# Kernel optimization log

Measured on AMD Instinct MI355X. Metric: run time of the kernel, lower is better.

## Reference

```python
import jax, jax.numpy as jnp
import numpy as np

D_MODEL = 1024
N_HEADS = 16
HEAD_DIM = D_MODEL // N_HEADS
D_LATENT = 256
LAMBDA_DECAY = 0.01
TIME_STEP = 0.01  # get_timestamps spacing; wall-clock base cancels in diffs
CLAMP = 1e4


def setup_inputs() -> dict:
    key = jax.random.key(0)
    ks = jax.random.split(key, 8)
    B, S = 2, 2048
    def w(k, i, o):
        return jax.random.normal(k, (i, o), dtype=jnp.float32) * 0.02
    return {
        "x": jax.random.normal(ks[0], (B, S, D_MODEL), dtype=jnp.float32),
        "Wq": w(ks[1], D_MODEL, D_MODEL),
        "Wk": w(ks[2], D_MODEL, D_MODEL),
        "Wv": w(ks[3], D_MODEL, D_MODEL),
        "Wo": w(ks[4], D_MODEL, D_MODEL),
        "W_down_kv": w(ks[5], D_MODEL, D_LATENT),
        "W_up_k": w(ks[6], D_LATENT, D_MODEL),
        "W_up_v": w(ks[7], D_LATENT, D_MODEL),
    }


def reference(x, Wq, Wk, Wv, Wo, W_down_kv, W_up_k, W_up_v):
    B, S, _ = x.shape
    q = x @ Wq
    k = x @ Wk
    v = x @ Wv
    latent_kv = (k + v) @ W_down_kv            # [B,S,d_latent]
    k_rec = latent_kv @ W_up_k                 # [B,S,d_model]
    v_rec = latent_kv @ W_up_v
    # split heads -> [B,H,S,hd]
    def heads(t):
        return t.reshape(B, S, N_HEADS, HEAD_DIM).transpose(0, 2, 1, 3)
    qh, kh, vh = heads(q), heads(k_rec), heads(v_rec)
    scale = 1.0 / (jnp.sqrt(jnp.float32(D_MODEL)) + 1e-8)
    scores = jnp.einsum("bhqd,bhkd->bhqk", qh, kh) * scale
    scores = jnp.clip(jnp.nan_to_num(scores, nan=-1e9), -CLAMP, CLAMP)
    # time decay: |t_i - t_j| = TIME_STEP * |i - j| (wall-clock base cancels)
    idx = jnp.arange(S, dtype=jnp.float32)
    decay = jnp.exp(-LAMBDA_DECAY * TIME_STEP * jnp.abs(idx[:, None] - idx[None, :]))
    scores = scores * decay[None, None, :, :]
    scores = jnp.clip(jnp.nan_to_num(scores, nan=-1e9), -CLAMP, CLAMP)
    attn = jax.nn.softmax(scores, axis=-1)
    out = jnp.einsum("bhqk,bhkd->bhqd", attn, vh)
    out = out.transpose(0, 2, 1, 3).reshape(B, S, D_MODEL)
    return out @ Wo, latent_kv
```

## Files before the change

### kernel.cpp

```cpp
#include <hip/hip_runtime.h>
#include <hip/hip_bf16.h>
#include <cstdint>
#include <cstddef>

typedef __bf16 bf16;
typedef __bf16 bf16x8 __attribute__((ext_vector_type(8)));
typedef float f32x4 __attribute__((ext_vector_type(4)));

#define NB 2
#define SEQ 2048
#define DM 1024
#define MTOK 4096
#define DL 256
#define NH 16
#define HD 64

#define LOG2E 1.4426950408889634f

__device__ __forceinline__ void gload16(const void* g, void* l) {
  __builtin_amdgcn_global_load_lds((const __attribute__((address_space(1))) void*)g,
                                   (__attribute__((address_space(3))) void*)l, 16, 0, 0);
}
__device__ __forceinline__ float fast_exp2(float x) {
#if __has_builtin(__builtin_amdgcn_exp2f)
  return __builtin_amdgcn_exp2f(x);
#else
  float r; asm("v_exp_f32 %0, %1" : "=v"(r) : "v"(x)); return r;
#endif
}
__device__ __forceinline__ int xcd_swz(int orig, int nwg) {
  int x = orig & 7;
  int q = nwg >> 3, r = nwg & 7;
  int base = (x < r) ? x * (q + 1) : r * (q + 1) + (x - r) * q;
  return base + (orig >> 3);
}

__device__ __forceinline__ void transpose_dev(const float* __restrict__ in0,
                                              bf16* __restrict__ out, int R, int C,
                                              int c0, int r0, int tid, float (*tile)[33]) {
  int tx = tid & 31, ty = tid >> 5;
#pragma unroll
  for (int i = 0; i < 4; ++i) {
    int r = r0 + ty + 8 * i;
    tile[ty + 8 * i][tx] = in0[(size_t)r * C + c0 + tx];
  }
  __syncthreads();
  int c = tid >> 3, s = tid & 7;
  bf16 o4[4] __attribute__((aligned(8)));
#pragma unroll
  for (int j = 0; j < 4; ++j) o4[j] = (bf16)tile[4 * s + j][c];
  *reinterpret_cast<uint2*>(out + (size_t)(c0 + c) * R + r0 + 4 * s) =
      *reinterpret_cast<const uint2*>(o4);
}

__device__ __forceinline__ void cvt8_dev(const float* __restrict__ in, bf16* __restrict__ out,
                                         int blk, int tid) {
  int i = (blk * 256 + tid) * 8;
  float4 a = *reinterpret_cast<const float4*>(in + i);
  float4 b = *reinterpret_cast<const float4*>(in + i + 4);
  bf16 o[8] __attribute__((aligned(16)));
  o[0] = (bf16)a.x; o[1] = (bf16)a.y; o[2] = (bf16)a.z; o[3] = (bf16)a.w;
  o[4] = (bf16)b.x; o[5] = (bf16)b.y; o[6] = (bf16)b.z; o[7] = (bf16)b.w;
  *reinterpret_cast<uint4*>(out + i) = *reinterpret_cast<const uint4*>(o);
}

__device__ __forceinline__ void sum8_dev(const float* __restrict__ in0, const float* __restrict__ in1,
                                         bf16* __restrict__ out, int blk, int tid) {
  int i = (blk * 256 + tid) * 8;
  float4 a0 = *reinterpret_cast<const float4*>(in0 + i);
  float4 b0 = *reinterpret_cast<const float4*>(in0 + i + 4);
  float4 a1 = *reinterpret_cast<const float4*>(in1 + i);
  float4 b1 = *reinterpret_cast<const float4*>(in1 + i + 4);
  bf16 o[8] __attribute__((aligned(16)));
  o[0] = (bf16)(a0.x + a1.x); o[1] = (bf16)(a0.y + a1.y);
  o[2] = (bf16)(a0.z + a1.z); o[3] = (bf16)(a0.w + a1.w);
  o[4] = (bf16)(b0.x + b1.x); o[5] = (bf16)(b0.y + b1.y);
  o[6] = (bf16)(b0.z + b1.z); o[7] = (bf16)(b0.w + b1.w);
  *reinterpret_cast<uint4*>(out + i) = *reinterpret_cast<const uint4*>(o);
}

__global__ __launch_bounds__(256) void prep_kernel(const float* __restrict__ x,
                                                   const float* __restrict__ Wq,
                                                   const float* __restrict__ Wk,
                                                   const float* __restrict__ Wv,
                                                   const float* __restrict__ Wo,
                                                   const float* __restrict__ Wdn,
                                                   const float* __restrict__ Wuk,
                                                   const float* __restrict__ Wuv,
                                                   bf16* xbf, bf16* WqT, bf16* WoT, bf16* WdnT,
                                                   bf16* WukT, bf16* WuvT, bf16* Wkv) {
  __shared__ float tile[32][33];
  int id = blockIdx.x, tid = threadIdx.x;
  if (id < 2048) { cvt8_dev(x, xbf, id, tid); return; }
  id -= 2048;
  if (id < 512) { sum8_dev(Wk, Wv, Wkv, id, tid); return; }
  id -= 512;
  if (id < 1024) { transpose_dev(Wq, WqT, 1024, 1024, (id & 31) * 32, (id >> 5) * 32, tid, tile); return; }
  id -= 1024;
  if (id < 1024) { transpose_dev(Wo, WoT, 1024, 1024, (id & 31) * 32, (id >> 5) * 32, tid, tile); return; }
  id -= 1024;
  if (id < 256) { transpose_dev(Wdn, WdnT, 1024, 256, (id & 7) * 32, (id >> 3) * 32, tid, tile); return; }
  id -= 256;
  if (id < 256) { transpose_dev(Wuk, WukT, 256, 1024, (id & 31) * 32, (id >> 5) * 32, tid, tile); return; }
  id -= 256;
  transpose_dev(Wuv, WuvT, 256, 1024, (id & 31) * 32, (id >> 5) * 32, tid, tile);
}

template <int EPI>
__device__ __forceinline__ void gemm_core(const bf16* __restrict__ A, const bf16* __restrict__ Bt,
                                          bf16* __restrict__ O1, float* __restrict__ Of,
                                          int K, int bx, int by, bf16* As, bf16* Bs) {
  const int tid = threadIdx.x;
  const int lane = tid & 63;
  const int wv = tid >> 6;
  const int wr = wv >> 1, wc = wv & 1;
  const int row0 = bx * 128, col0 = by * 64;
  const int l15 = lane & 15;
  const int lg = lane >> 4;

  const int r0 = tid >> 3;
  const int ccs = (tid & 7) ^ (r0 & 7);
  const bf16* aS = A + (size_t)(row0 + r0) * K + ccs * 8;
  const bf16* bS = Bt + (size_t)(col0 + r0) * K + ccs * 8;
  const int dA = tid * 8;

#pragma unroll
  for (int i = 0; i < 4; ++i) gload16(aS + (size_t)(32 * i) * K, As + dA + 2048 * i);
#pragma unroll
  for (int j = 0; j < 2; ++j) gload16(bS + (size_t)(32 * j) * K, Bs + dA + 2048 * j);
  aS += 64; bS += 64;

  int aoff[4][2], boff[2][2];
#pragma unroll
  for (int m = 0; m < 4; ++m) {
    int ra = wr * 64 + m * 16 + l15;
#pragma unroll
    for (int kk = 0; kk < 2; ++kk)
      aoff[m][kk] = ra * 64 + (((kk * 4 + lg) ^ (ra & 7)) * 8);
  }
#pragma unroll
  for (int n = 0; n < 2; ++n) {
    int rb = wc * 32 + n * 16 + l15;
#pragma unroll
    for (int kk = 0; kk < 2; ++kk)
      boff[n][kk] = rb * 64 + (((kk * 4 + lg) ^ (rb & 7)) * 8);
  }

  f32x4 acc[4][2] = {};
  int cur = 0;
  for (int k0 = 0; k0 < K; k0 += 64) {
    __syncthreads();
    if (k0 + 64 < K) {
      const int nxA = (cur ^ 1) * 8192, nxB = (cur ^ 1) * 4096;
#pragma unroll
      for (int i = 0; i < 4; ++i) gload16(aS + (size_t)(32 * i) * K, As + nxA + dA + 2048 * i);
#pragma unroll
      for (int j = 0; j < 2; ++j) gload16(bS + (size_t)(32 * j) * K, Bs + nxB + dA + 2048 * j);
      aS += 64; bS += 64;
    }
    const bf16* Ab = As + cur * 8192;
    const bf16* Bb = Bs + cur * 4096;
    bf16x8 af[4][2], bfr[2][2];
#pragma unroll
    for (int m = 0; m < 4; ++m)
#pragma unroll
      for (int kk = 0; kk < 2; ++kk)
        af[m][kk] = *reinterpret_cast<const bf16x8*>(&Ab[aoff[m][kk]]);
#pragma unroll
    for (int n = 0; n < 2; ++n)
#pragma unroll
      for (int kk = 0; kk < 2; ++kk)
        bfr[n][kk] = *reinterpret_cast<const bf16x8*>(&Bb[boff[n][kk]]);
    __builtin_amdgcn_s_setprio(1);
#pragma unroll
    for (int kk = 0; kk < 2; ++kk)
#pragma unroll
      for (int m = 0; m < 4; ++m)
#pragma unroll
        for (int n = 0; n < 2; ++n)
          acc[m][n] = __builtin_amdgcn_mfma_f32_16x16x32_bf16(af[m][kk], bfr[n][kk], acc[m][n], 0, 0, 0);
    __builtin_amdgcn_s_setprio(0);
    cur ^= 1;
  }

  const int rbase = row0 + wr * 64 + (lane >> 4) * 4;
  const int cbase = col0 + wc * 32 + l15;
#pragma unroll
  for (int m = 0; m < 4; ++m) {
#pragma unroll
    for (int n = 0; n < 2; ++n) {
      const int cc = cbase + n * 16;
      if constexpr (EPI == 0) {
#pragma unroll
        for (int r = 0; r < 4; ++r)
          O1[(size_t)(rbase + m * 16 + r) * DM + cc] = (bf16)acc[m][n][r];
      } else if constexpr (EPI == 3) {
#pragma unroll
        for (int r = 0; r < 4; ++r)
          Of[(size_t)(rbase + m * 16 + r) * DM + cc] = acc[m][n][r];
      } else {
#pragma unroll
        for (int r = 0; r < 4; ++r)
          O1[(size_t)(rbase + m * 16 + r) * MTOK + cc] = (bf16)acc[m][n][r];
      }
    }
  }
}

__device__ __forceinline__ void gemm64_lat(const bf16* __restrict__ A, const bf16* __restrict__ Bt,
                                           bf16* __restrict__ O1, float* __restrict__ Of,
                                           int K, int bx, int by, bf16* As, bf16* Bs) {
  const int tid = threadIdx.x;
  const int lane = tid & 63;
  const int wv = tid >> 6;
  const int wr = wv >> 1, wc = wv & 1;
  const int row0 = bx * 64, col0 = by * 64;
  const int l15 = lane & 15;
  const int lg = lane >> 4;

  const int r0 = tid >> 3;
  const int ccs = (tid & 7) ^ (r0 & 7);
  const bf16* aS = A + (size_t)(row0 + r0) * K + ccs * 8;
  const bf16* bS = Bt + (size_t)(col0 + r0) * K + ccs * 8;
  const int dA = tid * 8;

#pragma unroll
  for (int j = 0; j < 2; ++j) {
    gload16(aS + (size_t)(32 * j) * K, As + dA + 2048 * j);
    gload16(bS + (size_t)(32 * j) * K, Bs + dA + 2048 * j);
  }
  aS += 64; bS += 64;

  int aoff[2][2], boff[2][2];
#pragma unroll
  for (int m = 0; m < 2; ++m) {
    int ra = wr * 32 + m * 16 + l15;
    int rb = wc * 32 + m * 16 + l15;
#pragma unroll
    for (int kk = 0; kk < 2; ++kk) {
      aoff[m][kk] = ra * 64 + (((kk * 4 + lg) ^ (ra & 7)) * 8);
      boff[m][kk] = rb * 64 + (((kk * 4 + lg) ^ (rb & 7)) * 8);
    }
  }

  f32x4 acc[2][2] = {};
  int cur = 0;
  for (int k0 = 0; k0 < K; k0 += 64) {
    __syncthreads();
    if (k0 + 64 < K) {
      const int nx = (cur ^ 1) * 4096;
#pragma unroll
      for (int j = 0; j < 2; ++j) {
        gload16(aS + (size_t)(32 * j) * K, As + nx + dA + 2048 * j);
        gload16(bS + (size_t)(32 * j) * K, Bs + nx + dA + 2048 * j);
      }
      aS += 64; bS += 64;
    }
    const bf16* Ab = As + cur * 4096;
    const bf16* Bb = Bs + cur * 4096;
    bf16x8 af[2][2], bfr[2][2];
#pragma unroll
    for (int m = 0; m < 2; ++m)
#pragma unroll
      for (int kk = 0; kk < 2; ++kk) {
        af[m][kk] = *reinterpret_cast<const bf16x8*>(&Ab[aoff[m][kk]]);
        bfr[m][kk] = *reinterpret_cast<const bf16x8*>(&Bb[boff[m][kk]]);
      }
    __builtin_amdgcn_s_setprio(1);
#pragma unroll
    for (int kk = 0; kk < 2; ++kk)
#pragma unroll
      for (int m = 0; m < 2; ++m)
#pragma unroll
        for (int n = 0; n < 2; ++n)
          acc[m][n] = __builtin_amdgcn_mfma_f32_16x16x32_bf16(af[m][kk], bfr[n][kk], acc[m][n], 0, 0, 0);
    __builtin_amdgcn_s_setprio(0);
    cur ^= 1;
  }

  const int rbase = row0 + wr * 32 + (lane >> 4) * 4;
  const int cbase = col0 + wc * 32 + l15;
#pragma unroll
  for (int m = 0; m < 2; ++m)
#pragma unroll
    for (int n = 0; n < 2; ++n)
#pragma unroll
      for (int r = 0; r < 4; ++r) {
        float v = acc[m][n][r];
        O1[(size_t)(rbase + m * 16 + r) * DL + (cbase + n * 16)] = (bf16)v;
        Of[(size_t)(rbase + m * 16 + r) * DL + (cbase + n * 16)] = v;
      }
}

__global__ __launch_bounds__(256) void gemm_q_w(const bf16* __restrict__ xbf,
                                                const bf16* __restrict__ WqT, bf16* qbf,
                                                const bf16* __restrict__ WdnT,
                                                const bf16* __restrict__ Wkv, bf16* WkvdT) {
  __shared__ __align__(16) bf16 As[2 * 8192];
  __shared__ __align__(16) bf16 Bs[2 * 4096];
  int id = xcd_swz(blockIdx.x, 544);
  if (id < 32)
    gemm_core<0>(WdnT, Wkv, WkvdT, nullptr, DM, id >> 4, id & 15, As, Bs);
  else {
    int j = id - 32;
    gemm_core<0>(xbf, WqT, qbf, nullptr, DM, j >> 4, j & 15, As, Bs);
  }
}

__global__ __launch_bounds__(256) void gemm_latent(const bf16* __restrict__ xbf,
                                                   const bf16* __restrict__ WkvdT,
                                                   bf16* latbf, float* out_lat) {
  __shared__ __align__(16) bf16 As[2 * 4096];
  __shared__ __align__(16) bf16 Bs[2 * 4096];
  int id = xcd_swz(blockIdx.x, 256);
  gemm64_lat(xbf, WkvdT, latbf, out_lat, DM, id >> 2, id & 3, As, Bs);
}

__global__ __launch_bounds__(256) void gemm_up(const bf16* __restrict__ latbf,
                                               const bf16* __restrict__ WukT,
                                               const bf16* __restrict__ WuvT,
                                               bf16* kbuf, bf16* vT) {
  __shared__ __align__(16) bf16 As[2 * 8192];
  __shared__ __align__(16) bf16 Bs[2 * 4096];
  int id = xcd_swz(blockIdx.x, 1024);
  if (id < 512)
    gemm_core<0>(latbf, WukT, kbuf, nullptr, DL, id >> 4, id & 15, As, Bs);
  else {
    int j = id - 512;
    gemm_core<7>(WuvT, latbf, vT, nullptr, DL, j >> 6, j & 63, As, Bs);
  }
}

__global__ __launch_bounds__(256) void gemm_out(const bf16* __restrict__ ctx,
                                                const bf16* __restrict__ WoT, float* out0) {
  __shared__ __align__(16) bf16 As[2 * 8192];
  __shared__ __align__(16) bf16 Bs[2 * 4096];
  int id = xcd_swz(blockIdx.x, 512);
  gemm_core<3>(ctx, WoT, nullptr, out0, DM, id >> 4, id & 15, As, Bs);
}

__global__ __launch_bounds__(512) void attn_kernel(const bf16* __restrict__ Q,
                                                   const bf16* __restrict__ Kr,
                                                   const bf16* __restrict__ Vt,
                                                   bf16* __restrict__ Ctx) {
  __shared__ __align__(16) bf16 Ks[2 * 4096];
  __shared__ __align__(16) bf16 Vs[2 * 4096];
  __shared__ __align__(16) bf16 Ps[8192];
  const int work = xcd_swz(blockIdx.x, SEQ / 128 * NH * NB);
  const int qt = work & 15, h = (work >> 4) & 15, b = work >> 8;
  const int tid = threadIdx.x, lane = tid & 63, wv = tid >> 6;
  const int l15 = lane & 15, lg = lane >> 4;
  const int qbase = qt * 128 + wv * 16;
  const size_t tok0 = (size_t)b * SEQ;

  bf16x8 qf[2];
  {
    const bf16* qp = Q + (tok0 + qbase + l15) * DM + h * HD + lg * 8;
    qf[0] = *reinterpret_cast<const bf16x8*>(qp);
    qf[1] = *reinterpret_cast<const bf16x8*>(qp + 32);
  }

  const int r0s = tid >> 3;
  const int cc0 = (tid & 7) ^ (r0s & 7);
  const bf16* kS0 = Kr + (tok0 + r0s) * DM + h * HD + cc0 * 8;
  const bf16* vS0 = Vt + (size_t)(h * HD + r0s) * MTOK + tok0 + cc0 * 8;
  const int d0 = tid * 8;

  gload16(kS0, Ks + d0);
  gload16(vS0, Vs + d0);
  kS0 += 64 * DM; vS0 += 64;

  int koff[2][4], poffw[4], poffr[2];
  const int hsw = l15 & 7;
#pragma unroll
  for (int ks = 0; ks < 2; ++ks)
#pragma unroll
    for (int nf = 0; nf < 4; ++nf) {
      int row = nf * 16 + l15;
      koff[ks][nf] = row * 64 + (((ks * 4 + lg) ^ (row & 7)) * 8);
    }
  const int psBase = wv * 1024 + l15 * 64;
#pragma unroll
  for (int nf = 0; nf < 4; ++nf)
    poffw[nf] = psBase + (((nf * 2 + (lg >> 1)) ^ hsw) * 8) + (lg & 1) * 4;
#pragma unroll
  for (int ks = 0; ks < 2; ++ks)
    poffr[ks] = psBase + (((ks * 4 + lg) ^ hsw) * 8);

  bf16x8 ones;
#pragma unroll
  for (int j = 0; j < 8; ++j) ones[j] = (bf16)1.0f;

  f32x4 oacc[4] = {};
  f32x4 lacc = {};
  float dec[4][4];
  const float DEC2C = (1.0f / 32.0f) * LOG2E;
  const float NC2 = -1.0e-4f * LOG2E;
  const float E64 = 0.99362048f, IE64 = 1.00642051f;
  const int ib = -qbase - l15 + lg * 4;

  int cur = 0;
  for (int t = 0; t < SEQ / 64; ++t) {
    const int key0 = t * 64;
    __syncthreads();
    if (t + 1 < SEQ / 64) {
      const int nx = (cur ^ 1) * 4096;
      gload16(kS0, Ks + nx + d0);
      gload16(vS0, Vs + nx + d0);
      kS0 += 64 * DM; vS0 += 64;
    }
    {
      bool before = (key0 + 63 < qbase);
      bool afterp = (key0 >= qbase + 79);
      if (t == 0 || (!before && !afterp)) {
#pragma unroll
        for (int nf = 0; nf < 4; ++nf)
#pragma unroll
          for (int r = 0; r < 4; ++r) {
            float df = (float)(key0 + ib + nf * 16 + r);
            dec[nf][r] = DEC2C * fast_exp2(NC2 * fabsf(df));
          }
      } else {
        float mlt = before ? IE64 : E64;
#pragma unroll
        for (int nf = 0; nf < 4; ++nf)
#pragma unroll
          for (int r = 0; r < 4; ++r) dec[nf][r] *= mlt;
      }
    }
    const int kb = cur * 4096;

    f32x4 sc[4] = {};
    __builtin_amdgcn_s_setprio(1);
#pragma unroll
    for (int ks = 0; ks < 2; ++ks)
#pragma unroll
      for (int nf = 0; nf < 4; ++nf) {
        bf16x8 kf = *reinterpret_cast<const bf16x8*>(&Ks[kb + koff[ks][nf]]);
        sc[nf] = __builtin_amdgcn_mfma_f32_16x16x32_bf16(kf, qf[ks], sc[nf], 0, 0, 0);
      }
    __builtin_amdgcn_s_setprio(0);

#pragma unroll
    for (int nf = 0; nf < 4; ++nf) {
      bf16 t4[4] __attribute__((aligned(8)));
#pragma unroll
      for (int r = 0; r < 4; ++r) t4[r] = (bf16)fast_exp2(sc[nf][r] * dec[nf][r]);
      *reinterpret_cast<uint2*>(&Ps[poffw[nf]]) = *reinterpret_cast<const uint2*>(t4);
    }
    bf16x8 pb[2];
    pb[0] = *reinterpret_cast<const bf16x8*>(&Ps[poffr[0]]);
    pb[1] = *reinterpret_cast<const bf16x8*>(&Ps[poffr[1]]);

    __builtin_amdgcn_s_setprio(1);
#pragma unroll
    for (int ks = 0; ks < 2; ++ks) {
#pragma unroll
      for (int nf = 0; nf < 4; ++nf) {
        bf16x8 vf = *reinterpret_cast<const bf16x8*>(&Vs[kb + koff[ks][nf]]);
        oacc[nf] = __builtin_amdgcn_mfma_f32_16x16x32_bf16(vf, pb[ks], oacc[nf], 0, 0, 0);
      }
      lacc = __builtin_amdgcn_mfma_f32_16x16x32_bf16(ones, pb[ks], lacc, 0, 0, 0);
    }
    __builtin_amdgcn_s_setprio(0);
    cur ^= 1;
  }

  const float inv = 1.0f / lacc[0];
#pragma unroll
  for (int nf = 0; nf < 4; ++nf) {
    bf16 o4[4] __attribute__((aligned(8)));
#pragma unroll
    for (int r = 0; r < 4; ++r) o4[r] = (bf16)(oacc[nf][r] * inv);
    *reinterpret_cast<uint2*>(Ctx + (tok0 + qbase + l15) * DM + h * HD + nf * 16 + lg * 4) =
        *reinterpret_cast<const uint2*>(o4);
  }
}

extern "C" void kernel_launch(void* const* d_in, const int* in_sizes, int n_in,
                              void* d_out, int out_size, void* d_ws, size_t ws_size,
                              hipStream_t stream) {
  const float* x   = (const float*)d_in[0];
  const float* Wq  = (const float*)d_in[1];
  const float* Wk  = (const float*)d_in[2];
  const float* Wv  = (const float*)d_in[3];
  const float* Wo  = (const float*)d_in[4];
  const float* Wdn = (const float*)d_in[5];
  const float* Wuk = (const float*)d_in[6];
  const float* Wuv = (const float*)d_in[7];
  float* out0 = (float*)d_out;
  float* out_lat = out0 + (size_t)MTOK * DM;

  char* ws = (char*)d_ws;
  const size_t MB = 1u << 20;
  bf16* xbf   = (bf16*)(ws + 0);
  bf16* qbf   = (bf16*)(ws + 8 * MB);
  bf16* kbuf  = (bf16*)(ws + 16 * MB);
  bf16* Wkv   = kbuf;
  bf16* WkvdT = (bf16*)(ws + 18 * MB);
  bf16* vT    = (bf16*)(ws + 24 * MB);
  bf16* latbf = (bf16*)(ws + 32 * MB);
  bf16* WqT   = (bf16*)(ws + 34 * MB);
  bf16* WoT   = (bf16*)(ws + 36 * MB);
  bf16* WukT  = (bf16*)(ws + 38 * MB);
  bf16* WuvT  = (bf16*)(ws + 38 * MB + 512 * 1024);
  bf16* WdnT  = (bf16*)(ws + 39 * MB);
  bf16* ctx   = xbf;

  prep_kernel<<<5376, 256, 0, stream>>>(x, Wq, Wk, Wv, Wo, Wdn, Wuk, Wuv,
                                        xbf, WqT, WoT, WdnT, WukT, WuvT, Wkv);
  gemm_q_w<<<544, 256, 0, stream>>>(xbf, WqT, qbf, WdnT, Wkv, WkvdT);
  gemm_latent<<<256, 256, 0, stream>>>(xbf, WkvdT, latbf, out_lat);
  gemm_up<<<1024, 256, 0, stream>>>(latbf, WukT, WuvT, kbuf, vT);
  attn_kernel<<<512, 512, 0, stream>>>(qbf, kbuf, vT, ctx);
  gemm_out<<<512, 256, 0, stream>>>(ctx, WoT, out0);

  (void)in_sizes; (void)n_in; (void)out_size; (void)ws_size;
}
```

Before: 115.4 us.

## Fuse Q and latent projections into one GEMM over concatenated weights; 64x64 transposes

WkvdT is now written directly after WqT in the workspace, so a single 128x64-tile GEMM over 1280 output columns produces both Q and the latent. Its epilogue sends columns past 1024 to the bf16 latent and fp32 latent outputs. The small Wdn·Wkv product moves to its own 32-block launch ahead of it, which serializes a poorly occupied kernel that previously ran alongside the Q GEMM. The weight transposes in prep switch to 64x64 tiles with float4 loads and 16-byte stores, reducing block count and giving wider memory accesses.

```diff
diff --git a/kernel.cpp b/kernel.cpp
--- a/kernel.cpp
+++ b/kernel.cpp
@@ -35,22 +35,27 @@
   return base + (orig >> 3);
 }
 
-__device__ __forceinline__ void transpose_dev(const float* __restrict__ in0,
-                                              bf16* __restrict__ out, int R, int C,
-                                              int c0, int r0, int tid, float (*tile)[33]) {
-  int tx = tid & 31, ty = tid >> 5;
+__device__ __forceinline__ void transpose64_dev(const float* __restrict__ in0,
+                                                bf16* __restrict__ out, int R, int C,
+                                                int c0, int r0, int tid, float (*tile)[65]) {
+  int tx = tid & 15, ty = tid >> 4;
 #pragma unroll
   for (int i = 0; i < 4; ++i) {
-    int r = r0 + ty + 8 * i;
-    tile[ty + 8 * i][tx] = in0[(size_t)r * C + c0 + tx];
+    int r = r0 + ty + 16 * i;
+    float4 v = *reinterpret_cast<const float4*>(in0 + (size_t)r * C + c0 + tx * 4);
+    tile[ty + 16 * i][tx * 4 + 0] = v.x;
+    tile[ty + 16 * i][tx * 4 + 1] = v.y;
+    tile[ty + 16 * i][tx * 4 + 2] = v.z;
+    tile[ty + 16 * i][tx * 4 + 3] = v.w;
   }
   __syncthreads();
-  int c = tid >> 3, s = tid & 7;
-  bf16 o4[4] __attribute__((aligned(8)));
-#pragma unroll
-  for (int j = 0; j < 4; ++j) o4[j] = (bf16)tile[4 * s + j][c];
-  *reinterpret_cast<uint2*>(out + (size_t)(c0 + c) * R + r0 + 4 * s) =
-      *reinterpret_cast<const uint2*>(o4);
+  int c = tid >> 2, s = tid & 3;
+  bf16 o16[16] __attribute__((aligned(16)));
+#pragma unroll
+  for (int m = 0; m < 16; ++m) o16[m] = (bf16)tile[s * 16 + m][c];
+  uint4* dst = reinterpret_cast<uint4*>(out + (size_t)(c0 + c) * R + r0 + s * 16);
+  dst[0] = *reinterpret_cast<const uint4*>(o16);
+  dst[1] = *reinterpret_cast<const uint4*>(o16 + 8);
 }
 
 __device__ __forceinline__ void cvt8_dev(const float* __restrict__ in, bf16* __restrict__ out,
@@ -89,26 +94,27 @@
                                                    const float* __restrict__ Wuv,
                                                    bf16* xbf, bf16* WqT, bf16* WoT, bf16* WdnT,
                                                    bf16* WukT, bf16* WuvT, bf16* Wkv) {
-  __shared__ float tile[32][33];
+  __shared__ float tile[64][65];
   int id = blockIdx.x, tid = threadIdx.x;
   if (id < 2048) { cvt8_dev(x, xbf, id, tid); return; }
   id -= 2048;
   if (id < 512) { sum8_dev(Wk, Wv, Wkv, id, tid); return; }
   id -= 512;
-  if (id < 1024) { transpose_dev(Wq, WqT, 1024, 1024, (id & 31) * 32, (id >> 5) * 32, tid, tile); return; }
-  id -= 1024;
-  if (id < 1024) { transpose_dev(Wo, WoT, 1024, 1024, (id & 31) * 32, (id >> 5) * 32, tid, tile); return; }
-  id -= 1024;
-  if (id < 256) { transpose_dev(Wdn, WdnT, 1024, 256, (id & 7) * 32, (id >> 3) * 32, tid, tile); return; }
+  if (id < 256) { transpose64_dev(Wq, WqT, 1024, 1024, (id & 15) * 64, (id >> 4) * 64, tid, tile); return; }
   id -= 256;
-  if (id < 256) { transpose_dev(Wuk, WukT, 256, 1024, (id & 31) * 32, (id >> 5) * 32, tid, tile); return; }
+  if (id < 256) { transpose64_dev(Wo, WoT, 1024, 1024, (id & 15) * 64, (id >> 4) * 64, tid, tile); return; }
   id -= 256;
-  transpose_dev(Wuv, WuvT, 256, 1024, (id & 31) * 32, (id >> 5) * 32, tid, tile);
+  if (id < 64) { transpose64_dev(Wdn, WdnT, 1024, 256, (id & 3) * 64, (id >> 2) * 64, tid, tile); return; }
+  id -= 64;
+  if (id < 64) { transpose64_dev(Wuk, WukT, 256, 1024, (id & 15) * 64, (id >> 4) * 64, tid, tile); return; }
+  id -= 64;
+  transpose64_dev(Wuv, WuvT, 256, 1024, (id & 15) * 64, (id >> 4) * 64, tid, tile);
 }
 
 template <int EPI>
 __device__ __forceinline__ void gemm_core(const bf16* __restrict__ A, const bf16* __restrict__ Bt,
-                                          bf16* __restrict__ O1, float* __restrict__ Of,
+                                          bf16* __restrict__ O1, bf16* __restrict__ O2,
+                                          float* __restrict__ Of,
                                           int K, int bx, int by, bf16* As, bf16* Bs) {
   const int tid = threadIdx.x;
   const int lane = tid & 63;
@@ -198,6 +204,20 @@
 #pragma unroll
         for (int r = 0; r < 4; ++r)
           Of[(size_t)(rbase + m * 16 + r) * DM + cc] = acc[m][n][r];
+      } else if constexpr (EPI == 5) {
+        if (cc < 1024) {
+#pragma unroll
+          for (int r = 0; r < 4; ++r)
+            O1[(size_t)(rbase + m * 16 + r) * DM + cc] = (bf16)acc[m][n][r];
+        } else {
+          const int lcc = cc - 1024;
+#pragma unroll
+          for (int r = 0; r < 4; ++r) {
+            float v = acc[m][n][r];
+            O2[(size_t)(rbase + m * 16 + r) * DL + lcc] = (bf16)v;
+            Of[(size_t)(rbase + m * 16 + r) * DL + lcc] = v;
+          }
+        }
       } else {
 #pragma unroll
         for (int r = 0; r < 4; ++r)
@@ -207,113 +227,21 @@
   }
 }
 
-__device__ __forceinline__ void gemm64_lat(const bf16* __restrict__ A, const bf16* __restrict__ Bt,
-                                           bf16* __restrict__ O1, float* __restrict__ Of,
-                                           int K, int bx, int by, bf16* As, bf16* Bs) {
-  const int tid = threadIdx.x;
-  const int lane = tid & 63;
-  const int wv = tid >> 6;
-  const int wr = wv >> 1, wc = wv & 1;
-  const int row0 = bx * 64, col0 = by * 64;
-  const int l15 = lane & 15;
-  const int lg = lane >> 4;
-
-  const int r0 = tid >> 3;
-  const int ccs = (tid & 7) ^ (r0 & 7);
-  const bf16* aS = A + (size_t)(row0 + r0) * K + ccs * 8;
-  const bf16* bS = Bt + (size_t)(col0 + r0) * K + ccs * 8;
-  const int dA = tid * 8;
-
-#pragma unroll
-  for (int j = 0; j < 2; ++j) {
-    gload16(aS + (size_t)(32 * j) * K, As + dA + 2048 * j);
-    gload16(bS + (size_t)(32 * j) * K, Bs + dA + 2048 * j);
-  }
-  aS += 64; bS += 64;
-
-  int aoff[2][2], boff[2][2];
-#pragma unroll
-  for (int m = 0; m < 2; ++m) {
-    int ra = wr * 32 + m * 16 + l15;
-    int rb = wc * 32 + m * 16 + l15;
-#pragma unroll
-    for (int kk = 0; kk < 2; ++kk) {
-      aoff[m][kk] = ra * 64 + (((kk * 4 + lg) ^ (ra & 7)) * 8);
-      boff[m][kk] = rb * 64 + (((kk * 4 + lg) ^ (rb & 7)) * 8);
-    }
-  }
-
-  f32x4 acc[2][2] = {};
-  int cur = 0;
-  for (int k0 = 0; k0 < K; k0 += 64) {
-    __syncthreads();
-    if (k0 + 64 < K) {
-      const int nx = (cur ^ 1) * 4096;
-#pragma unroll
-      for (int j = 0; j < 2; ++j) {
-        gload16(aS + (size_t)(32 * j) * K, As + nx + dA + 2048 * j);
-        gload16(bS + (size_t)(32 * j) * K, Bs + nx + dA + 2048 * j);
-      }
-      aS += 64; bS += 64;
-    }
-    const bf16* Ab = As + cur * 4096;
-    const bf16* Bb = Bs + cur * 4096;
-    bf16x8 af[2][2], bfr[2][2];
-#pragma unroll
-    for (int m = 0; m < 2; ++m)
-#pragma unroll
-      for (int kk = 0; kk < 2; ++kk) {
-        af[m][kk] = *reinterpret_cast<const bf16x8*>(&Ab[aoff[m][kk]]);
-        bfr[m][kk] = *reinterpret_cast<const bf16x8*>(&Bb[boff[m][kk]]);
-      }
-    __builtin_amdgcn_s_setprio(1);
-#pragma unroll
-    for (int kk = 0; kk < 2; ++kk)
-#pragma unroll
-      for (int m = 0; m < 2; ++m)
-#pragma unroll
-        for (int n = 0; n < 2; ++n)
-          acc[m][n] = __builtin_amdgcn_mfma_f32_16x16x32_bf16(af[m][kk], bfr[n][kk], acc[m][n], 0, 0, 0);
-    __builtin_amdgcn_s_setprio(0);
-    cur ^= 1;
-  }
-
-  const int rbase = row0 + wr * 32 + (lane >> 4) * 4;
-  const int cbase = col0 + wc * 32 + l15;
-#pragma unroll
-  for (int m = 0; m < 2; ++m)
-#pragma unroll
-    for (int n = 0; n < 2; ++n)
-#pragma unroll
-      for (int r = 0; r < 4; ++r) {
-        float v = acc[m][n][r];
-        O1[(size_t)(rbase + m * 16 + r) * DL + (cbase + n * 16)] = (bf16)v;
-        Of[(size_t)(rbase + m * 16 + r) * DL + (cbase + n * 16)] = v;
-      }
-}
-
-__global__ __launch_bounds__(256) void gemm_q_w(const bf16* __restrict__ xbf,
-                                                const bf16* __restrict__ WqT, bf16* qbf,
-                                                const bf16* __restrict__ WdnT,
-                                                const bf16* __restrict__ Wkv, bf16* WkvdT) {
+__global__ __launch_bounds__(256) void gemm_wkvd(const bf16* __restrict__ WdnT,
+                                                 const bf16* __restrict__ Wkv, bf16* WkvdT) {
   __shared__ __align__(16) bf16 As[2 * 8192];
   __shared__ __align__(16) bf16 Bs[2 * 4096];
-  int id = xcd_swz(blockIdx.x, 544);
-  if (id < 32)
-    gemm_core<0>(WdnT, Wkv, WkvdT, nullptr, DM, id >> 4, id & 15, As, Bs);
-  else {
-    int j = id - 32;
-    gemm_core<0>(xbf, WqT, qbf, nullptr, DM, j >> 4, j & 15, As, Bs);
-  }
-}
-
-__global__ __launch_bounds__(256) void gemm_latent(const bf16* __restrict__ xbf,
-                                                   const bf16* __restrict__ WkvdT,
-                                                   bf16* latbf, float* out_lat) {
-  __shared__ __align__(16) bf16 As[2 * 4096];
+  int id = xcd_swz(blockIdx.x, 32);
+  gemm_core<0>(WdnT, Wkv, WkvdT, nullptr, nullptr, DM, id >> 4, id & 15, As, Bs);
+}
+
+__global__ __launch_bounds__(256) void gemm_qlat(const bf16* __restrict__ xbf,
+                                                 const bf16* __restrict__ Bq,
+                                                 bf16* qbf, bf16* latbf, float* out_lat) {
+  __shared__ __align__(16) bf16 As[2 * 8192];
   __shared__ __align__(16) bf16 Bs[2 * 4096];
-  int id = xcd_swz(blockIdx.x, 256);
-  gemm64_lat(xbf, WkvdT, latbf, out_lat, DM, id >> 2, id & 3, As, Bs);
+  int id = xcd_swz(blockIdx.x, 640);
+  gemm_core<5>(xbf, Bq, qbf, latbf, out_lat, DM, id / 20, id % 20, As, Bs);
 }
 
 __global__ __launch_bounds__(256) void gemm_up(const bf16* __restrict__ latbf,
@@ -324,10 +252,10 @@
   __shared__ __align__(16) bf16 Bs[2 * 4096];
   int id = xcd_swz(blockIdx.x, 1024);
   if (id < 512)
-    gemm_core<0>(latbf, WukT, kbuf, nullptr, DL, id >> 4, id & 15, As, Bs);
+    gemm_core<0>(latbf, WukT, kbuf, nullptr, nullptr, DL, id >> 4, id & 15, As, Bs);
   else {
     int j = id - 512;
-    gemm_core<7>(WuvT, latbf, vT, nullptr, DL, j >> 6, j & 63, As, Bs);
+    gemm_core<7>(WuvT, latbf, vT, nullptr, nullptr, DL, j >> 6, j & 63, As, Bs);
   }
 }
 
@@ -336,7 +264,7 @@
   __shared__ __align__(16) bf16 As[2 * 8192];
   __shared__ __align__(16) bf16 Bs[2 * 4096];
   int id = xcd_swz(blockIdx.x, 512);
-  gemm_core<3>(ctx, WoT, nullptr, out0, DM, id >> 4, id & 15, As, Bs);
+  gemm_core<3>(ctx, WoT, nullptr, nullptr, out0, DM, id >> 4, id & 15, As, Bs);
 }
 
 __global__ __launch_bounds__(512) void attn_kernel(const bf16* __restrict__ Q,
@@ -497,20 +425,20 @@
   bf16* qbf   = (bf16*)(ws + 8 * MB);
   bf16* kbuf  = (bf16*)(ws + 16 * MB);
   bf16* Wkv   = kbuf;
-  bf16* WkvdT = (bf16*)(ws + 18 * MB);
   bf16* vT    = (bf16*)(ws + 24 * MB);
   bf16* latbf = (bf16*)(ws + 32 * MB);
   bf16* WqT   = (bf16*)(ws + 34 * MB);
-  bf16* WoT   = (bf16*)(ws + 36 * MB);
-  bf16* WukT  = (bf16*)(ws + 38 * MB);
-  bf16* WuvT  = (bf16*)(ws + 38 * MB + 512 * 1024);
-  bf16* WdnT  = (bf16*)(ws + 39 * MB);
+  bf16* WkvdT = (bf16*)(ws + 36 * MB);
+  bf16* WoT   = (bf16*)(ws + 36 * MB + 512 * 1024);
+  bf16* WukT  = (bf16*)(ws + 38 * MB + 512 * 1024);
+  bf16* WuvT  = (bf16*)(ws + 39 * MB);
+  bf16* WdnT  = (bf16*)(ws + 39 * MB + 512 * 1024);
   bf16* ctx   = xbf;
 
-  prep_kernel<<<5376, 256, 0, stream>>>(x, Wq, Wk, Wv, Wo, Wdn, Wuk, Wuv,
+  prep_kernel<<<3264, 256, 0, stream>>>(x, Wq, Wk, Wv, Wo, Wdn, Wuk, Wuv,
                                         xbf, WqT, WoT, WdnT, WukT, WuvT, Wkv);
-  gemm_q_w<<<544, 256, 0, stream>>>(xbf, WqT, qbf, WdnT, Wkv, WkvdT);
-  gemm_latent<<<256, 256, 0, stream>>>(xbf, WkvdT, latbf, out_lat);
+  gemm_wkvd<<<32, 256, 0, stream>>>(WdnT, Wkv, WkvdT);
+  gemm_qlat<<<640, 256, 0, stream>>>(xbf, WqT, qbf, latbf, out_lat);
   gemm_up<<<1024, 256, 0, stream>>>(latbf, WukT, WuvT, kbuf, vT);
   attn_kernel<<<512, 512, 0, stream>>>(qbf, kbuf, vT, ctx);
   gemm_out<<<512, 256, 0, stream>>>(ctx, WoT, out0);
```

Result: slower. 120.9 us (+4.7%).
